# Optimization experiments

Hardware: AMD Instinct MI355X
Metric: run time of the kernel (lower is better)

The kernel has to match this reference:

```python
import jax, jax.numpy as jnp
import numpy as np
from jax import lax

# Conv3d(in_dim, in_dim, kernel=(1,3,3), padding=(0,1,1)) == per-time-slice 3x3 conv mixing channels

def _conv3d(x, w, b):
    # x: [B, C, T, W, H], w: [O, I, 1, 3, 3], b: [O]
    y = lax.conv_general_dilated(
        x, w,
        window_strides=(1, 1, 1),
        padding=[(0, 0), (1, 1), (1, 1)],
        dimension_numbers=("NCDHW", "OIDHW", "NCDHW"),
    )
    return y + b[None, :, None, None, None]


def setup_inputs() -> dict:
    key = jax.random.key(0)
    ks = jax.random.split(key, 8)
    B, C, T, W, H = 8, 64, 16, 64, 64
    fan = C * 1 * 3 * 3
    bound = 1.0 / np.sqrt(fan)  # torch Conv3d default init range
    x = jax.random.normal(ks[0], (B, C, T, W, H), dtype=jnp.float32)
    wq = jax.random.uniform(ks[1], (C, C, 1, 3, 3), jnp.float32, -bound, bound)
    wk = jax.random.uniform(ks[2], (C, C, 1, 3, 3), jnp.float32, -bound, bound)
    wv = jax.random.uniform(ks[3], (C, C, 1, 3, 3), jnp.float32, -bound, bound)
    bq = jax.random.uniform(ks[4], (C,), jnp.float32, -bound, bound)
    bk = jax.random.uniform(ks[5], (C,), jnp.float32, -bound, bound)
    bv = jax.random.uniform(ks[6], (C,), jnp.float32, -bound, bound)
    # torch init is gamma=0 (identity output); use nonzero so reference exercises the full path
    gamma = jax.random.normal(ks[7], (1,), dtype=jnp.float32) * 0.1
    return {"x": x, "wq": wq, "wk": wk, "wv": wv,
            "bq": bq, "bk": bk, "bv": bv, "gamma": gamma}


def reference(x, wq, wk, wv, bq, bk, bv, gamma):
    B, C, T, W, H = x.shape
    WH = W * H
    q = _conv3d(x, wq, bq).reshape(B, C, T, WH)
    k = _conv3d(x, wk, bk).reshape(B, C, T, WH)
    v = _conv3d(x, wv, bv).reshape(B, C, T, WH)
    # Original: (q[...,:,None] @ k[...,None,:]) @ v[...,:,None]  -> rank-1 energy, no softmax.
    # Exact reassociation: out_i = q_i * sum_j(k_j * v_j), avoiding the [WH, WH] matrix.
    s = jnp.sum(k * v, axis=-1, keepdims=True)  # [B, C, T, 1]
    out = (q * s).reshape(B, C, T, W, H)
    return gamma[0] * out + x
```

## Files before the change

### kernel.cpp

```cpp
#include <hip/hip_runtime.h>
#include <hip/hip_bf16.h>
#include <stdint.h>

typedef __attribute__((ext_vector_type(8))) short bf16x8;
typedef __attribute__((ext_vector_type(4))) float f32x4v;
typedef __attribute__((ext_vector_type(16))) float f32x16;

#define CH_STRIDE 65536

__device__ __forceinline__ uint16_t f2bf(float f) {
  uint32_t u = __builtin_bit_cast(uint32_t, f);
  u = (u + 0x7FFFu + ((u >> 16) & 1u)) >> 16;
  return (uint16_t)u;
}
__device__ __forceinline__ float bf2f(uint32_t b) {
  return __builtin_bit_cast(float, b << 16);
}
__device__ __forceinline__ uint16_t cvt_bf(float f) {
  return __builtin_bit_cast(uint16_t, __float2bfloat16(f));
}

#define MFMA32(a, b, c) __builtin_amdgcn_mfma_f32_32x32x16_bf16(a, b, c, 0, 0, 0)
#define LGKM0 asm volatile("s_waitcnt lgkmcnt(0)" ::: "memory")
#define BAR __builtin_amdgcn_s_barrier()
#define SCHED0 __builtin_amdgcn_sched_barrier(0)

#define LDSX_BYTES (6 * 8 * 66 * 16)

__device__ __forceinline__ uint32_t swz(uint32_t b) {
  return b ^ (((b >> 7) & 7u) << 4);
}

__device__ __forceinline__ bf16x8 ldx(const uint8_t* ldsx, int r6, int oct, int ci) {
  return *(const bf16x8*)(ldsx + swz((uint32_t)((r6 * 8 + oct) * 66 + ci) * 16u));
}

__device__ __forceinline__ void stage_unit(uint8_t* ldsx, const float* xs, int w0, int u) {
  int r6 = u >> 7, oct = (u >> 4) & 7, g = u & 15;
  int w = w0 - 1 + r6;
  uint32_t base = (uint32_t)((r6 * 8 + oct) * 66 + 4 * g + 1) * 16u;
  if ((unsigned)w < 64u) {
    const float* p = xs + (size_t)(oct * 8) * CH_STRIDE + w * 64 + 4 * g;
    f32x4v v[8];
    #pragma unroll
    for (int j = 0; j < 8; ++j) v[j] = *(const f32x4v*)(p + (size_t)j * CH_STRIDE);
    #pragma unroll
    for (int c = 0; c < 4; ++c) {
      bf16x8 frag;
      #pragma unroll
      for (int q = 0; q < 4; ++q) {
        frag[2 * q]     = (short)cvt_bf(v[2 * q][c]);
        frag[2 * q + 1] = (short)cvt_bf(v[2 * q + 1][c]);
      }
      *(bf16x8*)(ldsx + swz(base + (uint32_t)c * 16u)) = frag;
    }
  } else {
    bf16x8 z = {};
    #pragma unroll
    for (int c = 0; c < 4; ++c)
      *(bf16x8*)(ldsx + swz(base + (uint32_t)c * 16u)) = z;
  }
}
__device__ __forceinline__ void stage_halo(uint8_t* ldsx, int tid) {
  if (tid < 96) {
    int r6 = tid >> 4, rem = tid & 15;
    int oct = rem >> 1, side = rem & 1;
    bf16x8 z = {};
    *(bf16x8*)(ldsx + swz((uint32_t)((r6 * 8 + oct) * 66 + side * 65) * 16u)) = z;
  }
}
__device__ __forceinline__ void stage_x256(uint8_t* ldsx, const float* xs, int w0, int tid) {
  stage_halo(ldsx, tid);
  #pragma unroll
  for (int k = 0; k < 3; ++k) stage_unit(ldsx, xs, w0, tid + k * 256);
}
__device__ __forceinline__ void stage_x512(uint8_t* ldsx, const float* xs, int w0, int tid) {
  stage_halo(ldsx, tid);
  stage_unit(ldsx, xs, w0, tid);
  if (tid < 256) stage_unit(ldsx, xs, w0, 512 + tid);
}

__device__ __forceinline__ bf16x8 ldw_kv(const uint8_t* ldsw, int oct, int rowloc) {
  return *(const bf16x8*)(ldsw + (uint32_t)(oct * 128 + rowloc) * 16u);
}
__device__ __forceinline__ void ldw_g_kv2(bf16x8* r, const uint16_t* wkv, int tap, int tid) {
  #pragma unroll
  for (int k = 0; k < 2; ++k)
    r[k] = *(const bf16x8*)(wkv + ((size_t)tap * 1024 + tid + k * 512) * 8);
}
__device__ __forceinline__ void stw_kv2(uint8_t* ldsw, const bf16x8* r, int tid) {
  #pragma unroll
  for (int k = 0; k < 2; ++k)
    *(bf16x8*)(ldsw + (uint32_t)(tid + k * 512) * 16u) = r[k];
}

__device__ __forceinline__ bf16x8 ldw_q(const uint8_t* ldsw, int oct, int row) {
  return *(const bf16x8*)(ldsw + (uint32_t)(oct * 64 + row) * 16u);
}
__device__ __forceinline__ void ldw_g_q(bf16x8* r, const uint16_t* wq, int tap, int tid) {
  #pragma unroll
  for (int k = 0; k < 2; ++k)
    r[k] = *(const bf16x8*)(wq + ((size_t)tap * 512 + tid + k * 256) * 8);
}
__device__ __forceinline__ void stw_q(uint8_t* ldsw, const bf16x8* r, int tid) {
  #pragma unroll
  for (int k = 0; k < 2; ++k)
    *(bf16x8*)(ldsw + (uint32_t)(tid + k * 256) * 16u) = r[k];
}

__global__ void prep_weights(const float* __restrict__ wq, const float* __restrict__ wk,
                             const float* __restrict__ wv, uint16_t* __restrict__ wout) {
  int i = blockIdx.x * 256 + threadIdx.x;
  if (i >= 110592) return;
  if (i < 36864) {
    int tap = i >> 12, oct = (i >> 9) & 7, row = (i >> 3) & 63, j = i & 7;
    wout[i] = f2bf(wq[(row * 64 + oct * 8 + j) * 9 + tap]);
  } else {
    int m = i - 36864;
    int tap = m >> 13, oct = (m >> 10) & 7, rl = (m >> 3) & 127, j = m & 7;
    const float* src = (rl < 64) ? wk : wv;
    wout[i] = f2bf(src[((rl & 63) * 64 + oct * 8 + j) * 9 + tap]);
  }
}

__global__ __launch_bounds__(512, 4) void kv_s_kernel(
    const float* __restrict__ x, const uint16_t* __restrict__ wkv,
    const float* __restrict__ bk, const float* __restrict__ bv,
    float* __restrict__ s_out) {
  extern __shared__ uint8_t lds[];
  uint8_t* ldsx = lds;
  uint8_t* ldsw = lds + LDSX_BYTES;
  const int tid = threadIdx.x;
  const int l = tid & 63;
  const int wid = tid >> 6;
  const int ng = wid & 3, mg = wid >> 2;
  int bid = (int)(blockIdx.x & 7) * 256 + (int)(blockIdx.x >> 3);
  const int rg = bid & 15, slice = bid >> 4;
  const int b = slice >> 4, t = slice & 15;
  const int w0 = rg * 4;
  const float* xs = x + ((size_t)b * 1024 + t) * 4096;
  const int lm = l & 31, lh = l >> 5;

  stage_x512(ldsx, xs, w0, tid);
  bf16x8 r[2];
  ldw_g_kv2(r, wkv, 0, tid);
  stw_kv2(ldsw, r, tid);
  ldw_g_kv2(r, wkv, 1, tid);
  SCHED0; LGKM0; BAR; SCHED0;

  f32x16 accK[2], accV[2];
  #pragma unroll
  for (int nt = 0; nt < 2; ++nt)
    #pragma unroll
    for (int q = 0; q < 16; ++q) { accK[nt][q] = 0.f; accV[nt][q] = 0.f; }

  #pragma unroll
  for (int tap = 0; tap < 9; ++tap) {
    const int dy = tap / 3, dx = tap % 3;
    __builtin_amdgcn_s_setprio(1);
    #pragma unroll
    for (int s = 0; s < 4; ++s) {
      int oct = s * 2 + lh;
      bf16x8 aK = ldw_kv(ldsw, oct, mg * 32 + lm);
      bf16x8 aV = ldw_kv(ldsw, oct, 64 + mg * 32 + lm);
      bf16x8 b0 = ldx(ldsx, ng + dy, oct, lm + dx);
      bf16x8 b1 = ldx(ldsx, ng + dy, oct, 32 + lm + dx);
      accK[0] = MFMA32(aK, b0, accK[0]);
      accK[1] = MFMA32(aK, b1, accK[1]);
      accV[0] = MFMA32(aV, b0, accV[0]);
      accV[1] = MFMA32(aV, b1, accV[1]);
    }
    __builtin_amdgcn_s_setprio(0);
    if (tap < 8) {
      SCHED0; BAR;
      stw_kv2(ldsw, r, tid);
      if (tap < 7) ldw_g_kv2(r, wkv, tap + 2, tid);
      SCHED0; LGKM0; BAR; SCHED0;
    }
  }

  __syncthreads();
  float* red = (float*)lds;
  #pragma unroll
  for (int q = 0; q < 16; ++q) {
    int cl = (q & 3) + 8 * (q >> 2) + 4 * lh;
    int c = mg * 32 + cl;
    float bkc = bk[c], bvc = bv[c];
    float p = (accK[0][q] + bkc) * (accV[0][q] + bvc)
            + (accK[1][q] + bkc) * (accV[1][q] + bvc);
    red[c * 132 + ng * 32 + lm] = p;
  }
  __syncthreads();
  if (tid < 64) {
    const f32x4v* rp = (const f32x4v*)(red + tid * 132);
    f32x4v a4 = {0.f, 0.f, 0.f, 0.f};
    #pragma unroll
    for (int j = 0; j < 32; ++j) a4 += rp[j];
    atomicAdd(s_out + (b * 16 + t) * 64 + tid, a4[0] + a4[1] + a4[2] + a4[3]);
  }
}

__global__ __launch_bounds__(256, 2) void q_out_kernel(
    const float* __restrict__ x, const uint16_t* __restrict__ wq,
    const float* __restrict__ bq, const float* __restrict__ s_in,
    const float* __restrict__ gamma, float* __restrict__ out) {
  extern __shared__ uint8_t lds[];
  uint8_t* ldsx = lds;
  uint8_t* ldsw = lds + LDSX_BYTES;
  const int tid = threadIdx.x;
  const int l = tid & 63, ng = tid >> 6;
  int bid = (int)(blockIdx.x & 7) * 256 + (int)(blockIdx.x >> 3);
  const int rg = bid & 15, slice = bid >> 4;
  const int b = slice >> 4, t = slice & 15;
  const int w0 = rg * 4;
  const float* xs = x + ((size_t)b * 1024 + t) * 4096;
  const int lm = l & 31, lh = l >> 5;

  stage_x256(ldsx, xs, w0, tid);
  bf16x8 r[2];
  ldw_g_q(r, wq, 0, tid);
  stw_q(ldsw, r, tid);
  ldw_g_q(r, wq, 1, tid);
  SCHED0; LGKM0; BAR; SCHED0;

  f32x16 acc[2][2];
  #pragma unroll
  for (int mt = 0; mt < 2; ++mt)
    #pragma unroll
    for (int nt = 0; nt < 2; ++nt)
      #pragma unroll
      for (int q = 0; q < 16; ++q) acc[mt][nt][q] = 0.f;

  #pragma unroll
  for (int tap = 0; tap < 9; ++tap) {
    const int dy = tap / 3, dx = tap % 3;
    __builtin_amdgcn_s_setprio(1);
    #pragma unroll
    for (int s = 0; s < 4; ++s) {
      int oct = s * 2 + lh;
      bf16x8 a0 = ldw_q(ldsw, oct, lm);
      bf16x8 a1 = ldw_q(ldsw, oct, 32 + lm);
      bf16x8 b0 = ldx(ldsx, ng + dy, oct, lm + dx);
      bf16x8 b1 = ldx(ldsx, ng + dy, oct, 32 + lm + dx);
      acc[0][0] = MFMA32(a0, b0, acc[0][0]);
      acc[0][1] = MFMA32(a0, b1, acc[0][1]);
      acc[1][0] = MFMA32(a1, b0, acc[1][0]);
      acc[1][1] = MFMA32(a1, b1, acc[1][1]);
    }
    __builtin_amdgcn_s_setprio(0);
    if (tap < 8) {
      SCHED0; BAR;
      stw_q(ldsw, r, tid);
      if (tap < 7) ldw_g_q(r, wq, tap + 2, tid);
      SCHED0; LGKM0; BAR; SCHED0;
    }
  }

  float g = gamma[0];
  const float* sb = s_in + (b * 16 + t) * 64;
  int w = w0 + ng;
  #pragma unroll
  for (int mt = 0; mt < 2; ++mt) {
    #pragma unroll
    for (int q = 0; q < 16; ++q) {
      int cl = (q & 3) + 8 * (q >> 2) + 4 * lh;
      int c  = mt * 32 + cl;
      float qb = bq[c], sc = sb[c];
      #pragma unroll
      for (int nt = 0; nt < 2; ++nt) {
        int h = nt * 32 + lm;
        uint32_t xb = (uint32_t)(((ng + 1) * 8 + (c >> 3)) * 66 + (h + 1)) * 16u
                    + (uint32_t)(c & 7) * 2u;
        float xv = bf2f(*(const uint16_t*)(ldsx + swz(xb)));
        size_t idx = ((size_t)(b * 64 + c) * 16 + t) * 4096 + (size_t)w * 64 + h;
        out[idx] = g * (acc[mt][nt][q] + qb) * sc + xv;
      }
    }
  }
}

extern "C" void kernel_launch(void* const* d_in, const int* in_sizes, int n_in,
                              void* d_out, int out_size, void* d_ws, size_t ws_size,
                              hipStream_t stream) {
  const float* x   = (const float*)d_in[0];
  const float* wq  = (const float*)d_in[1];
  const float* wk  = (const float*)d_in[2];
  const float* wv  = (const float*)d_in[3];
  const float* bq  = (const float*)d_in[4];
  const float* bk  = (const float*)d_in[5];
  const float* bv  = (const float*)d_in[6];
  const float* gam = (const float*)d_in[7];

  uint16_t* wbf = (uint16_t*)d_ws;
  float* sbuf   = (float*)((uint8_t*)d_ws + 221184);

  hipMemsetAsync(sbuf, 0, 8 * 16 * 64 * sizeof(float), stream);
  prep_weights<<<(110592 + 255) / 256, 256, 0, stream>>>(wq, wk, wv, wbf);
  kv_s_kernel<<<2048, 512, LDSX_BYTES + 16384, stream>>>(x, wbf + 36864, bk, bv, sbuf);
  q_out_kernel<<<2048, 256, LDSX_BYTES + 8192, stream>>>(x, wbf, bq, sbuf, gam, (float*)d_out);
}
```

Baseline: 156.5 us.

## Double the kv tile to 1024-thread blocks with double-buffered weight taps

```diff
diff --git a/kernel.cpp b/kernel.cpp
--- a/kernel.cpp
+++ b/kernel.cpp
@@ -25,20 +25,21 @@
 #define BAR __builtin_amdgcn_s_barrier()
 #define SCHED0 __builtin_amdgcn_sched_barrier(0)
 
-#define LDSX_BYTES (6 * 8 * 66 * 16)
+#define LDSX6  (6 * 8 * 66 * 16)
+#define LDSX10 (10 * 8 * 66 * 16)
 
 __device__ __forceinline__ uint32_t swz(uint32_t b) {
   return b ^ (((b >> 7) & 7u) << 4);
 }
 
-__device__ __forceinline__ bf16x8 ldx(const uint8_t* ldsx, int r6, int oct, int ci) {
-  return *(const bf16x8*)(ldsx + swz((uint32_t)((r6 * 8 + oct) * 66 + ci) * 16u));
+__device__ __forceinline__ bf16x8 ldx(const uint8_t* ldsx, int row, int oct, int ci) {
+  return *(const bf16x8*)(ldsx + swz((uint32_t)((row * 8 + oct) * 66 + ci) * 16u));
 }
 
 __device__ __forceinline__ void stage_unit(uint8_t* ldsx, const float* xs, int w0, int u) {
-  int r6 = u >> 7, oct = (u >> 4) & 7, g = u & 15;
-  int w = w0 - 1 + r6;
-  uint32_t base = (uint32_t)((r6 * 8 + oct) * 66 + 4 * g + 1) * 16u;
+  int row = u >> 7, oct = (u >> 4) & 7, g = u & 15;
+  int w = w0 - 1 + row;
+  uint32_t base = (uint32_t)((row * 8 + oct) * 66 + 4 * g + 1) * 16u;
   if ((unsigned)w < 64u) {
     const float* p = xs + (size_t)(oct * 8) * CH_STRIDE + w * 64 + 4 * g;
     f32x4v v[8];
@@ -61,39 +62,28 @@
       *(bf16x8*)(ldsx + swz(base + (uint32_t)c * 16u)) = z;
   }
 }
-__device__ __forceinline__ void stage_halo(uint8_t* ldsx, int tid) {
-  if (tid < 96) {
-    int r6 = tid >> 4, rem = tid & 15;
+__device__ __forceinline__ void stage_halo(uint8_t* ldsx, int tid, int nrow) {
+  if (tid < nrow * 16) {
+    int row = tid >> 4, rem = tid & 15;
     int oct = rem >> 1, side = rem & 1;
     bf16x8 z = {};
-    *(bf16x8*)(ldsx + swz((uint32_t)((r6 * 8 + oct) * 66 + side * 65) * 16u)) = z;
+    *(bf16x8*)(ldsx + swz((uint32_t)((row * 8 + oct) * 66 + side * 65) * 16u)) = z;
   }
 }
 __device__ __forceinline__ void stage_x256(uint8_t* ldsx, const float* xs, int w0, int tid) {
-  stage_halo(ldsx, tid);
+  stage_halo(ldsx, tid, 6);
   #pragma unroll
   for (int k = 0; k < 3; ++k) stage_unit(ldsx, xs, w0, tid + k * 256);
 }
-__device__ __forceinline__ void stage_x512(uint8_t* ldsx, const float* xs, int w0, int tid) {
-  stage_halo(ldsx, tid);
+__device__ __forceinline__ void stage_x1024(uint8_t* ldsx, const float* xs, int w0, int tid) {
+  stage_halo(ldsx, tid, 10);
   stage_unit(ldsx, xs, w0, tid);
-  if (tid < 256) stage_unit(ldsx, xs, w0, 512 + tid);
+  if (tid < 256) stage_unit(ldsx, xs, w0, 1024 + tid);
 }
 
 __device__ __forceinline__ bf16x8 ldw_kv(const uint8_t* ldsw, int oct, int rowloc) {
   return *(const bf16x8*)(ldsw + (uint32_t)(oct * 128 + rowloc) * 16u);
 }
-__device__ __forceinline__ void ldw_g_kv2(bf16x8* r, const uint16_t* wkv, int tap, int tid) {
-  #pragma unroll
-  for (int k = 0; k < 2; ++k)
-    r[k] = *(const bf16x8*)(wkv + ((size_t)tap * 1024 + tid + k * 512) * 8);
-}
-__device__ __forceinline__ void stw_kv2(uint8_t* ldsw, const bf16x8* r, int tid) {
-  #pragma unroll
-  for (int k = 0; k < 2; ++k)
-    *(bf16x8*)(ldsw + (uint32_t)(tid + k * 512) * 16u) = r[k];
-}
-
 __device__ __forceinline__ bf16x8 ldw_q(const uint8_t* ldsw, int oct, int row) {
   return *(const bf16x8*)(ldsw + (uint32_t)(oct * 64 + row) * 16u);
 }
@@ -123,29 +113,30 @@
   }
 }
 
-__global__ __launch_bounds__(512, 4) void kv_s_kernel(
+__global__ __launch_bounds__(1024, 4) void kv_s_kernel(
     const float* __restrict__ x, const uint16_t* __restrict__ wkv,
     const float* __restrict__ bk, const float* __restrict__ bv,
     float* __restrict__ s_out) {
   extern __shared__ uint8_t lds[];
   uint8_t* ldsx = lds;
-  uint8_t* ldsw = lds + LDSX_BYTES;
+  uint8_t* ldswA = lds + LDSX10;
+  uint8_t* ldswB = lds + LDSX10 + 16384;
   const int tid = threadIdx.x;
   const int l = tid & 63;
   const int wid = tid >> 6;
-  const int ng = wid & 3, mg = wid >> 2;
-  int bid = (int)(blockIdx.x & 7) * 256 + (int)(blockIdx.x >> 3);
-  const int rg = bid & 15, slice = bid >> 4;
+  const int ng = wid & 7, mg = wid >> 3;
+  int bid = (int)(blockIdx.x & 7) * 128 + (int)(blockIdx.x >> 3);
+  const int rg = bid & 7, slice = bid >> 3;
   const int b = slice >> 4, t = slice & 15;
-  const int w0 = rg * 4;
+  const int w0 = rg * 8;
   const float* xs = x + ((size_t)b * 1024 + t) * 4096;
   const int lm = l & 31, lh = l >> 5;
 
-  stage_x512(ldsx, xs, w0, tid);
-  bf16x8 r[2];
-  ldw_g_kv2(r, wkv, 0, tid);
-  stw_kv2(ldsw, r, tid);
-  ldw_g_kv2(r, wkv, 1, tid);
+  stage_x1024(ldsx, xs, w0, tid);
+  bf16x8 r_pref;
+  r_pref = *(const bf16x8*)(wkv + (size_t)tid * 8);
+  *(bf16x8*)(ldswA + (uint32_t)tid * 16u) = r_pref;
+  r_pref = *(const bf16x8*)(wkv + ((size_t)1024 + tid) * 8);
   SCHED0; LGKM0; BAR; SCHED0;
 
   f32x16 accK[2], accV[2];
@@ -157,26 +148,37 @@
   #pragma unroll
   for (int tap = 0; tap < 9; ++tap) {
     const int dy = tap / 3, dx = tap % 3;
+    const uint8_t* bufc = (tap & 1) ? ldswB : ldswA;
+    uint8_t* bufn = (tap & 1) ? ldswA : ldswB;
+    int oct0 = lh;
+    bf16x8 aK = ldw_kv(bufc, oct0, mg * 32 + lm);
+    bf16x8 aV = ldw_kv(bufc, oct0, 64 + mg * 32 + lm);
+    bf16x8 b0 = ldx(ldsx, ng + dy, oct0, lm + dx);
+    bf16x8 b1 = ldx(ldsx, ng + dy, oct0, 32 + lm + dx);
+    if (tap < 8) {
+      *(bf16x8*)(bufn + (uint32_t)tid * 16u) = r_pref;
+      if (tap < 7)
+        r_pref = *(const bf16x8*)(wkv + ((size_t)(tap + 2) * 1024 + tid) * 8);
+    }
     __builtin_amdgcn_s_setprio(1);
-    #pragma unroll
-    for (int s = 0; s < 4; ++s) {
+    accK[0] = MFMA32(aK, b0, accK[0]);
+    accK[1] = MFMA32(aK, b1, accK[1]);
+    accV[0] = MFMA32(aV, b0, accV[0]);
+    accV[1] = MFMA32(aV, b1, accV[1]);
+    #pragma unroll
+    for (int s = 1; s < 4; ++s) {
       int oct = s * 2 + lh;
-      bf16x8 aK = ldw_kv(ldsw, oct, mg * 32 + lm);
-      bf16x8 aV = ldw_kv(ldsw, oct, 64 + mg * 32 + lm);
-      bf16x8 b0 = ldx(ldsx, ng + dy, oct, lm + dx);
-      bf16x8 b1 = ldx(ldsx, ng + dy, oct, 32 + lm + dx);
+      aK = ldw_kv(bufc, oct, mg * 32 + lm);
+      aV = ldw_kv(bufc, oct, 64 + mg * 32 + lm);
+      b0 = ldx(ldsx, ng + dy, oct, lm + dx);
+      b1 = ldx(ldsx, ng + dy, oct, 32 + lm + dx);
       accK[0] = MFMA32(aK, b0, accK[0]);
       accK[1] = MFMA32(aK, b1, accK[1]);
       accV[0] = MFMA32(aV, b0, accV[0]);
       accV[1] = MFMA32(aV, b1, accV[1]);
     }
     __builtin_amdgcn_s_setprio(0);
-    if (tap < 8) {
-      SCHED0; BAR;
-      stw_kv2(ldsw, r, tid);
-      if (tap < 7) ldw_g_kv2(r, wkv, tap + 2, tid);
-      SCHED0; LGKM0; BAR; SCHED0;
-    }
+    SCHED0; LGKM0; BAR; SCHED0;
   }
 
   __syncthreads();
@@ -188,14 +190,14 @@
     float bkc = bk[c], bvc = bv[c];
     float p = (accK[0][q] + bkc) * (accV[0][q] + bvc)
             + (accK[1][q] + bkc) * (accV[1][q] + bvc);
-    red[c * 132 + ng * 32 + lm] = p;
+    red[c * 260 + ng * 32 + lm] = p;
   }
   __syncthreads();
   if (tid < 64) {
-    const f32x4v* rp = (const f32x4v*)(red + tid * 132);
+    const f32x4v* rp = (const f32x4v*)(red + tid * 260);
     f32x4v a4 = {0.f, 0.f, 0.f, 0.f};
     #pragma unroll
-    for (int j = 0; j < 32; ++j) a4 += rp[j];
+    for (int j = 0; j < 64; ++j) a4 += rp[j];
     atomicAdd(s_out + (b * 16 + t) * 64 + tid, a4[0] + a4[1] + a4[2] + a4[3]);
   }
 }
@@ -206,7 +208,7 @@
     const float* __restrict__ gamma, float* __restrict__ out) {
   extern __shared__ uint8_t lds[];
   uint8_t* ldsx = lds;
-  uint8_t* ldsw = lds + LDSX_BYTES;
+  uint8_t* ldsw = lds + LDSX6;
   const int tid = threadIdx.x;
   const int l = tid & 63, ng = tid >> 6;
   int bid = (int)(blockIdx.x & 7) * 256 + (int)(blockIdx.x >> 3);
@@ -296,6 +298,6 @@
 
   hipMemsetAsync(sbuf, 0, 8 * 16 * 64 * sizeof(float), stream);
   prep_weights<<<(110592 + 255) / 256, 256, 0, stream>>>(wq, wk, wv, wbf);
-  kv_s_kernel<<<2048, 512, LDSX_BYTES + 16384, stream>>>(x, wbf + 36864, bk, bv, sbuf);
-  q_out_kernel<<<2048, 256, LDSX_BYTES + 8192, stream>>>(x, wbf, bq, sbuf, gam, (float*)d_out);
-}
+  kv_s_kernel<<<1024, 1024, LDSX10 + 32768, stream>>>(x, wbf + 36864, bk, bv, sbuf);
+  q_out_kernel<<<2048, 256, LDSX6 + 8192, stream>>>(x, wbf, bq, sbuf, gam, (float*)d_out);
+}
```

After: 156.2 us. Within noise of the previous version (-0.2%).
